# Performance work log

Measured on AMD Instinct MI355X. Metric: run time of the kernel, lower is better.

## Reference

```python
import jax, jax.numpy as jnp
import numpy as np
import math

B, N, D, SEQ = 4, 1024, 512, 256
HID, DIST_D, N_NER, N_LAB = 150, 128, 3, 4
SPANS_PER_WORD = 0.5
ASPECT, OPINION = 1, 2
NUM_DIST_EMB = 512


def setup_inputs() -> dict:
    key = jax.random.key(0)
    ks = jax.random.split(key, 9)
    starts = jax.random.randint(ks[0], (B, N), 0, SEQ)
    widths = jax.random.randint(ks[1], (B, N), 0, 8)
    ends = jnp.clip(starts + widths, 0, SEQ - 1)
    spans = jnp.stack([starts, ends], axis=-1).astype(jnp.int32)  # [B,N,2]
    ner_scores = jax.random.normal(ks[2], (B, N, N_NER), jnp.float32)
    span_embeddings = jax.random.normal(ks[3], (B, N, D), jnp.float32)
    span_mask = jnp.ones((B, N), dtype=bool)

    pair_dim = 2 * D + DIST_D

    def xavier(k, shape):
        std = math.sqrt(2.0 / (shape[0] + shape[1]))
        return jax.random.normal(k, shape, jnp.float32) * std

    dist_table = xavier(ks[4], (NUM_DIST_EMB, DIST_D))
    W1 = xavier(ks[5], (pair_dim, HID)); b1 = jnp.zeros((HID,), jnp.float32)
    W2 = xavier(ks[6], (HID, HID));      b2 = jnp.zeros((HID,), jnp.float32)
    Wc = xavier(ks[7], (HID, N_LAB));    bc = jnp.zeros((N_LAB,), jnp.float32)

    return dict(spans=spans, ner_scores=ner_scores, span_embeddings=span_embeddings,
                span_mask=span_mask, seq_length=SEQ, dist_table=dist_table,
                W1=W1, b1=b1, W2=W2, b2=b2, Wc=Wc, bc=bc)


def bucket_values(d, num_identity=4, num_total=10):
    # semi-logscale buckets: [0,1,2,3,4,5-7,8-15,16-31,32-63,64+]
    logspace = jnp.floor(jnp.log2(jnp.maximum(d, 1).astype(jnp.float32))).astype(jnp.int32) + (num_identity - 1)
    return jnp.clip(jnp.where(d <= num_identity, d, logspace), 0, num_total - 1)


def _prune(scores, mask, k):
    masked = jnp.where(mask, scores, jnp.float32(-1e20))
    _, idx = jax.lax.top_k(masked, k)  # [B,k]
    return idx


def reference(spans, ner_scores, span_embeddings, span_mask, seq_length,
              dist_table, W1, b1, W2, b2, Wc, bc):
    bsz, n_spans, d = span_embeddings.shape
    k = min(int(math.ceil(seq_length * SPANS_PER_WORD)), n_spans)

    a_idx = _prune(ner_scores[..., ASPECT], span_mask, k)    # [B,k]
    o_idx = _prune(ner_scores[..., OPINION], span_mask, k)
    a_keep = jnp.ones((bsz, k), dtype=bool)  # uniform seq_length -> all kept
    o_keep = a_keep

    gather = lambda t, i: jnp.take_along_axis(t, i[..., None], axis=1)
    a_emb = gather(span_embeddings, a_idx)   # [B,k,D]
    o_emb = gather(span_embeddings, o_idx)   # [B,k,D]
    spans_a = gather(spans, a_idx)           # [B,k,2]
    spans_o = gather(spans, o_idx)           # [B,k,2]

    # pairwise min span distance -> bucket -> embedding
    dis1 = jnp.abs(spans_a[..., 0][:, :, None] - spans_o[..., 1][:, None, :])
    dis2 = jnp.abs(spans_a[..., 1][:, :, None] - spans_o[..., 0][:, None, :])
    dis = jnp.minimum(dis1, dis2)                      # [B,k,k]
    dist_emb = dist_table[bucket_values(dis)]          # [B,k,k,DIST_D]

    pair = jnp.concatenate([
        jnp.broadcast_to(a_emb[:, :, None, :], (bsz, k, k, d)),
        jnp.broadcast_to(o_emb[:, None, :, :], (bsz, k, k, d)),
        dist_emb,
    ], axis=-1)                                        # [B,k,k,2D+DIST_D]

    # FeedForward (2 layers, ReLU, dropout=identity at eval) + classifier
    h = jax.nn.relu(pair @ W1 + b1)
    h = jax.nn.relu(h @ W2 + b2)
    scores = h @ Wc + bc                               # [B,k,k,n_labels]

    rel_mask = a_keep[:, :, None] & o_keep[:, None, :]
    return (jax.nn.softmax(scores, axis=-1), rel_mask, pair, spans_a, spans_o)
```

## Files before the change

kernel.cpp:

```cpp
#include <hip/hip_runtime.h>
#include <hip/hip_bf16.h>

#define BB 4
#define NN 1024
#define DD 512
#define KK 128
#define HID 150
#define HIDP 160
#define W2TS 176
#define DIST_D 128
#define PAIRD 1152

typedef __attribute__((ext_vector_type(4))) float f32x4;
typedef __attribute__((ext_vector_type(8))) short s16x8;

__device__ __forceinline__ int bucket_of(int dd) {
    return (dd <= 4) ? dd : min(34 - __clz(dd), 9);
}

__global__ __launch_bounds__(256) void k_topk(const int* __restrict__ spans,
                                              const float* __restrict__ ner,
                                              const float* __restrict__ dist_table,
                                              const float* __restrict__ W1,
                                              const float* __restrict__ b1,
                                              const float* __restrict__ W2,
                                              int* ws_aidx, int* ws_oidx,
                                              int* ws_sa, int* ws_so,
                                              float* ws_cd, __hip_bfloat16* ws_w2t,
                                              float* out3, float* out4) {
    int t = threadIdx.x;
    int bx = blockIdx.x;
    if (bx < 32) {
        __shared__ unsigned long long sk[NN];
        int b = bx >> 3;
        int which = (bx >> 2) & 1;
        int chunk = bx & 3;
        int ch = which ? 2 : 1;
#pragma unroll
        for (int k = 0; k < 4; ++k) {
            int d = k * 256 + t;
            float v = ner[(b * NN + d) * 3 + ch];
            unsigned int u = __float_as_uint(v);
            unsigned int s = (u & 0x80000000u) ? ~u : (u ^ 0x80000000u);
            sk[d] = ((unsigned long long)s << 32) | (unsigned int)(NN - 1 - d);
        }
        __syncthreads();
        int idx = chunk * 256 + t;
        unsigned long long mine = sk[idx];
        int cnt = 0;
#pragma unroll 16
        for (int d = 0; d < NN; ++d) cnt += (sk[d] > mine) ? 1 : 0;
        if (cnt < KK) {
            int s0 = spans[(b * NN + idx) * 2];
            int s1 = spans[(b * NN + idx) * 2 + 1];
            int row = b * KK + cnt;
            if (which == 0) {
                ws_aidx[row] = idx;
                ws_sa[row * 2] = s0; ws_sa[row * 2 + 1] = s1;
                out3[row * 2] = (float)s0; out3[row * 2 + 1] = (float)s1;
            } else {
                ws_oidx[row] = idx;
                ws_so[row * 2] = s0; ws_so[row * 2 + 1] = s1;
                out4[row * 2] = (float)s0; out4[row * 2 + 1] = (float)s1;
            }
        }
    } else if (bx < 42) {
        int bk = bx - 32;
        if (t < HIDP) {
            float acc = 0.f;
            if (t < HID) {
                acc = b1[t];
                for (int d = 0; d < DIST_D; ++d)
                    acc = fmaf(dist_table[bk * DIST_D + d], W1[(size_t)(2 * DD + d) * HID + t], acc);
            }
            ws_cd[bk * HIDP + t] = acc;
        }
    } else {
        int e = (bx - 42) * 256 + t;
        if (e < HIDP * W2TS) {
            int n = e / W2TS, d = e - n * W2TS;
            float v = (n < HID && d < HID) ? W2[d * HID + n] : 0.f;
            ws_w2t[e] = __float2bfloat16(v);
        }
    }
}

__global__ __launch_bounds__(256) void k_prep(const float* __restrict__ emb,
                                              const float* __restrict__ W1,
                                              const int* __restrict__ ws_aidx,
                                              const int* __restrict__ ws_oidx,
                                              float* ws_ca, float* ws_co,
                                              float* ws_acomp, float* ws_ocomp,
                                              float* __restrict__ out1) {
    __shared__ __align__(16) float es[4][DD];
    int t = threadIdx.x;
    int bx = blockIdx.x;

    if (bx >= 384) {
        int i = (bx - 384) * 256 + t;
        ((float4*)out1)[i] = make_float4(1.f, 1.f, 1.f, 1.f);
        return;
    }
    if (bx >= 256) {
        int cb = bx - 256;
        int r0 = cb * 8;
        int c = t & 127;
        bool isA = r0 < 512;
        const int* idxsrc = isA ? ws_aidx : ws_oidx;
        float* dstc = isA ? ws_acomp : ws_ocomp;
        int base = isA ? r0 : r0 - 512;
#pragma unroll
        for (int rr = 0; rr < 8; rr += 2) {
            int brow = base + rr + (t >> 7);
            int b = brow >> 7;
            int idx = idxsrc[brow];
            f32x4 v = ((const f32x4*)(emb + ((size_t)(b * NN) + idx) * DD))[c];
            ((f32x4*)dstc)[(size_t)brow * 128 + c] = v;
        }
        return;
    }

    int which = bx >> 7;
    int row0 = (bx & 127) * 4;
    const int* idxsrc = which ? ws_oidx : ws_aidx;
    for (int x = t; x < 512; x += 256) {
        int r = x >> 7, c = x & 127;
        int row = row0 + r;
        int b = row >> 7;
        int idx = idxsrc[row];
        ((float4*)es[r])[c] = ((const float4*)(emb + ((size_t)(b * NN) + idx) * DD))[c];
    }
    __syncthreads();
    if (t < HIDP) {
        float a0 = 0.f, a1 = 0.f, a2 = 0.f, a3 = 0.f;
        if (t < HID) {
            const float* w = W1 + (size_t)(which * DD) * HID + t;
#pragma unroll 4
            for (int d4 = 0; d4 < 128; ++d4) {
                float4 e0 = ((const float4*)es[0])[d4];
                float4 e1 = ((const float4*)es[1])[d4];
                float4 e2 = ((const float4*)es[2])[d4];
                float4 e3 = ((const float4*)es[3])[d4];
                float w0 = w[(size_t)(4 * d4 + 0) * HID];
                float w1v = w[(size_t)(4 * d4 + 1) * HID];
                float w2v = w[(size_t)(4 * d4 + 2) * HID];
                float w3 = w[(size_t)(4 * d4 + 3) * HID];
                a0 = fmaf(e0.x, w0, a0); a0 = fmaf(e0.y, w1v, a0); a0 = fmaf(e0.z, w2v, a0); a0 = fmaf(e0.w, w3, a0);
                a1 = fmaf(e1.x, w0, a1); a1 = fmaf(e1.y, w1v, a1); a1 = fmaf(e1.z, w2v, a1); a1 = fmaf(e1.w, w3, a1);
                a2 = fmaf(e2.x, w0, a2); a2 = fmaf(e2.y, w1v, a2); a2 = fmaf(e2.z, w2v, a2); a2 = fmaf(e2.w, w3, a2);
                a3 = fmaf(e3.x, w0, a3); a3 = fmaf(e3.y, w1v, a3); a3 = fmaf(e3.z, w2v, a3); a3 = fmaf(e3.w, w3, a3);
            }
        }
        float* dstb = which ? ws_co : ws_ca;
        dstb[(row0 + 0) * HIDP + t] = a0;
        dstb[(row0 + 1) * HIDP + t] = a1;
        dstb[(row0 + 2) * HIDP + t] = a2;
        dstb[(row0 + 3) * HIDP + t] = a3;
    }
}

__global__ __launch_bounds__(256, 2) void k_fused(const float* __restrict__ dist_table,
                                                  const float* __restrict__ Wc,
                                                  const float* __restrict__ bcp,
                                                  const float* __restrict__ b2p,
                                                  const int* __restrict__ ws_sa,
                                                  const int* __restrict__ ws_so,
                                                  const float* __restrict__ ws_ca,
                                                  const float* __restrict__ ws_co,
                                                  const float* __restrict__ ws_cd,
                                                  const __hip_bfloat16* __restrict__ ws_w2t,
                                                  const float* __restrict__ ws_acomp,
                                                  const float* __restrict__ ws_ocomp,
                                                  float* __restrict__ out0,
                                                  float* __restrict__ out2) {
    int t = threadIdx.x;
    int bx = blockIdx.x;

    if (bx & 1) {
        int pid = bx >> 1;
        int b = pid >> 7;
        int ig = (pid >> 2) & 31;
        int jc = pid & 3;
        int i0 = ig << 2;
        int j0 = jc << 5;
        int c = t & 127;
        int half = t >> 7;

        const f32x4* abase = (const f32x4*)ws_acomp;
        const f32x4* obase = (const f32x4*)ws_ocomp;

        f32x4 areg[4];
#pragma unroll
        for (int ii = 0; ii < 4; ++ii)
            areg[ii] = abase[(size_t)(b * KK + i0 + ii) * 128 + c];

        f32x4 oreg[16];
#pragma unroll
        for (int it = 0; it < 16; ++it) {
            int j = it * 2 + half;
            oreg[it] = obase[(size_t)(b * KK + j0 + j) * 128 + c];
        }

        int dj[4], dc[4], so0v[4], so1v[4];
#pragma unroll
        for (int it = 0; it < 4; ++it) {
            int x = it * 256 + t;
            dj[it] = x >> 5; dc[it] = x & 31;
            so0v[it] = ws_so[(b * KK + j0 + dj[it]) * 2];
            so1v[it] = ws_so[(b * KK + j0 + dj[it]) * 2 + 1];
        }
        f32x4 dreg[4][4];
#pragma unroll
        for (int ii = 0; ii < 4; ++ii) {
            int sa0 = ws_sa[(b * KK + i0 + ii) * 2];
            int sa1 = ws_sa[(b * KK + i0 + ii) * 2 + 1];
#pragma unroll
            for (int it = 0; it < 4; ++it) {
                int bkt = bucket_of(min(abs(sa0 - so1v[it]), abs(sa1 - so0v[it])));
                dreg[ii][it] = ((const f32x4*)dist_table)[bkt * 32 + dc[it]];
            }
        }

#pragma unroll
        for (int ii = 0; ii < 4; ++ii) {
            f32x4* dst = (f32x4*)(out2 + (size_t)(b * KK + i0 + ii) * (KK * PAIRD))
                         + (size_t)j0 * 288;
#pragma unroll
            for (int it = 0; it < 16; ++it) {
                int j = it * 2 + half;
                dst[j * 288 + c] = areg[ii];
                dst[j * 288 + 128 + c] = oreg[it];
            }
#pragma unroll
            for (int it = 0; it < 4; ++it)
                dst[dj[it] * 288 + 256 + dc[it]] = dreg[ii][it];
        }
        return;
    }

    int bi = bx >> 1;
    int b = bi >> 7;
    int wave = t >> 6, l = t & 63;
    int lc = l & 15, lg = l >> 4;
    int r0 = wave * 32 + lc, r1 = r0 + 16;

    int sa0 = ws_sa[bi * 2], sa1 = ws_sa[bi * 2 + 1];
    int so00 = ws_so[(b * KK + r0) * 2], so01 = ws_so[(b * KK + r0) * 2 + 1];
    int so10 = ws_so[(b * KK + r1) * 2], so11 = ws_so[(b * KK + r1) * 2 + 1];
    int bkt0 = bucket_of(min(abs(sa0 - so01), abs(sa1 - so00)));
    int bkt1 = bucket_of(min(abs(sa0 - so11), abs(sa1 - so10)));

    const f32x4* ca4 = (const f32x4*)(ws_ca + (size_t)bi * HIDP);
    const f32x4* co04 = (const f32x4*)(ws_co + (size_t)(b * KK + r0) * HIDP);
    const f32x4* co14 = (const f32x4*)(ws_co + (size_t)(b * KK + r1) * HIDP);
    const f32x4* cd04 = (const f32x4*)(ws_cd + (size_t)bkt0 * HIDP);
    const f32x4* cd14 = (const f32x4*)(ws_cd + (size_t)bkt1 * HIDP);

    s16x8 af0[5], af1[5];
    union U8 { s16x8 frag; __hip_bfloat16 h[8]; };
#pragma unroll
    for (int kk = 0; kk < 5; ++kk) {
        int o = kk * 8 + lg * 2;
        f32x4 caa = ca4[o], cab = ca4[o + 1];
        f32x4 s0a = caa + co04[o] + cd04[o];
        f32x4 s0b = cab + co04[o + 1] + cd04[o + 1];
        f32x4 s1a = caa + co14[o] + cd14[o];
        f32x4 s1b = cab + co14[o + 1] + cd14[o + 1];
        U8 u0, u1;
#pragma unroll
        for (int e = 0; e < 4; ++e) {
            u0.h[e]     = __float2bfloat16(fmaxf(s0a[e], 0.f));
            u0.h[e + 4] = __float2bfloat16(fmaxf(s0b[e], 0.f));
            u1.h[e]     = __float2bfloat16(fmaxf(s1a[e], 0.f));
            u1.h[e + 4] = __float2bfloat16(fmaxf(s1b[e], 0.f));
        }
        af0[kk] = u0.frag;
        af1[kk] = u1.frag;
    }

    f32x4 acc[2][10];
#pragma unroll
    for (int mi = 0; mi < 2; ++mi)
#pragma unroll
        for (int nt = 0; nt < 10; ++nt)
            acc[mi][nt] = (f32x4){0.f, 0.f, 0.f, 0.f};

#pragma unroll
    for (int kk = 0; kk < 5; ++kk) {
#pragma unroll
        for (int nt = 0; nt < 10; ++nt) {
            s16x8 bf = *(const s16x8*)&ws_w2t[(nt * 16 + lc) * W2TS + kk * 32 + lg * 8];
            acc[0][nt] = __builtin_amdgcn_mfma_f32_16x16x32_bf16(af0[kk], bf, acc[0][nt], 0, 0, 0);
            acc[1][nt] = __builtin_amdgcn_mfma_f32_16x16x32_bf16(af1[kk], bf, acc[1][nt], 0, 0, 0);
        }
    }

    float4 wcv[10];
    float b2v[10];
#pragma unroll
    for (int nt = 0; nt < 10; ++nt) {
        int n = nt * 16 + lc;
        if (n < HID) {
            wcv[nt] = *(const float4*)(Wc + n * 4);
            b2v[nt] = b2p[n];
        } else {
            wcv[nt] = make_float4(0.f, 0.f, 0.f, 0.f);
            b2v[nt] = 0.f;
        }
    }
    float bc0 = bcp[0], bc1 = bcp[1], bc2 = bcp[2], bc3 = bcp[3];

#pragma unroll
    for (int mi = 0; mi < 2; ++mi) {
#pragma unroll
        for (int r = 0; r < 4; ++r) {
            int j = wave * 32 + mi * 16 + lg * 4 + r;
            float p0 = 0.f, p1 = 0.f, p2 = 0.f, p3 = 0.f;
#pragma unroll
            for (int nt = 0; nt < 10; ++nt) {
                float h2 = fmaxf(acc[mi][nt][r] + b2v[nt], 0.f);
                p0 = fmaf(h2, wcv[nt].x, p0);
                p1 = fmaf(h2, wcv[nt].y, p1);
                p2 = fmaf(h2, wcv[nt].z, p2);
                p3 = fmaf(h2, wcv[nt].w, p3);
            }
#pragma unroll
            for (int m = 8; m >= 1; m >>= 1) {
                p0 += __shfl_xor(p0, m, 16);
                p1 += __shfl_xor(p1, m, 16);
                p2 += __shfl_xor(p2, m, 16);
                p3 += __shfl_xor(p3, m, 16);
            }
            p0 += bc0; p1 += bc1; p2 += bc2; p3 += bc3;
            float mx = fmaxf(fmaxf(p0, p1), fmaxf(p2, p3));
            float e0 = expf(p0 - mx), e1 = expf(p1 - mx), e2 = expf(p2 - mx), e3 = expf(p3 - mx);
            float inv = 1.f / (e0 + e1 + e2 + e3);
            if (lc < 4) {
                float v = (lc == 0) ? e0 : (lc == 1) ? e1 : (lc == 2) ? e2 : e3;
                out0[((size_t)bi * KK + j) * 4 + lc] = v * inv;
            }
        }
    }
}

extern "C" void kernel_launch(void* const* d_in, const int* in_sizes, int n_in,
                              void* d_out, int out_size, void* d_ws, size_t ws_size,
                              hipStream_t stream) {
    const int*   spans = (const int*)d_in[0];
    const float* ner   = (const float*)d_in[1];
    const float* emb   = (const float*)d_in[2];
    const float* dist_table = (const float*)d_in[5];
    const float* W1 = (const float*)d_in[6];
    const float* b1 = (const float*)d_in[7];
    const float* W2 = (const float*)d_in[8];
    const float* b2 = (const float*)d_in[9];
    const float* Wc = (const float*)d_in[10];
    const float* bc = (const float*)d_in[11];

    float* out0 = (float*)d_out;
    float* out1 = out0 + (size_t)BB * KK * KK * 4;
    float* out2 = out1 + (size_t)BB * KK * KK;
    float* out3 = out2 + (size_t)BB * KK * KK * PAIRD;
    float* out4 = out3 + (size_t)BB * KK * 2;

    float* ws_acomp = (float*)d_ws;
    float* ws_ocomp = ws_acomp + 512 * 512;
    int* ws_aidx = (int*)(ws_ocomp + 512 * 512);
    int* ws_oidx = ws_aidx + BB * KK;
    int* ws_sa   = ws_oidx + BB * KK;
    int* ws_so   = ws_sa + BB * KK * 2;
    float* ws_ca = (float*)(ws_so + BB * KK * 2);
    float* ws_co = ws_ca + BB * KK * HIDP;
    float* ws_cd = ws_co + BB * KK * HIDP;
    __hip_bfloat16* ws_w2t = (__hip_bfloat16*)(ws_cd + 16 * HIDP);

    k_topk<<<152, 256, 0, stream>>>(spans, ner, dist_table, W1, b1, W2,
                                    ws_aidx, ws_oidx, ws_sa, ws_so,
                                    ws_cd, ws_w2t, out3, out4);
    k_prep<<<448, 256, 0, stream>>>(emb, W1, ws_aidx, ws_oidx,
                                    ws_ca, ws_co, ws_acomp, ws_ocomp, out1);
    k_fused<<<1024, 256, 0, stream>>>(dist_table, Wc, bc, b2,
                                      ws_sa, ws_so, ws_ca, ws_co, ws_cd, ws_w2t,
                                      ws_acomp, ws_ocomp, out0, out2);
}
```

Measured before the change: 96.99 us.

## Precompute distance buckets and flatten pair-tensor writes into strided grid loop

The distance bucket for every (i,j) pair is now computed once in k_prep blocks and stored in a workspace array. The pair-tensor writer in k_fused becomes a flat grid-stride loop in which each thread writes consecutive float4s. Element coordinates are recovered with multiply-shift division by 9. Writer blocks are interleaved 4:1 with MLP blocks (2560 blocks) instead of 1:1. The aim is fully coalesced streaming stores for the large pair output and better overlap with compute, at the cost of redundant, less-cached reads of the a/o/dist rows and per-element index arithmetic.

```diff
diff --git a/kernel.cpp b/kernel.cpp
--- a/kernel.cpp
+++ b/kernel.cpp
@@ -17,6 +17,8 @@
 __device__ __forceinline__ int bucket_of(int dd) {
     return (dd <= 4) ? dd : min(34 - __clz(dd), 9);
 }
+
+__device__ __forceinline__ int div9(int x) { return (x * 7282) >> 16; }
 
 __global__ __launch_bounds__(256) void k_topk(const int* __restrict__ spans,
                                               const float* __restrict__ ner,
@@ -89,16 +91,32 @@
                                               const float* __restrict__ W1,
                                               const int* __restrict__ ws_aidx,
                                               const int* __restrict__ ws_oidx,
+                                              const int* __restrict__ ws_sa,
+                                              const int* __restrict__ ws_so,
                                               float* ws_ca, float* ws_co,
                                               float* ws_acomp, float* ws_ocomp,
+                                              int* ws_bkt,
                                               float* __restrict__ out1) {
     __shared__ __align__(16) float es[4][DD];
     int t = threadIdx.x;
     int bx = blockIdx.x;
 
+    if (bx >= 448) {
+        int i = (bx - 448) * 256 + t;
+        ((float4*)out1)[i] = make_float4(1.f, 1.f, 1.f, 1.f);
+        return;
+    }
     if (bx >= 384) {
-        int i = (bx - 384) * 256 + t;
-        ((float4*)out1)[i] = make_float4(1.f, 1.f, 1.f, 1.f);
+        int cb = bx - 384;
+#pragma unroll
+        for (int k = 0; k < 4; ++k) {
+            int e = cb * 1024 + k * 256 + t;
+            int bi = e >> 7, j = e & 127;
+            int b = bi >> 7;
+            int sa0 = ws_sa[bi * 2], sa1 = ws_sa[bi * 2 + 1];
+            int so0 = ws_so[(b * KK + j) * 2], so1 = ws_so[(b * KK + j) * 2 + 1];
+            ws_bkt[e] = bucket_of(min(abs(sa0 - so1), abs(sa1 - so0)));
+        }
         return;
     }
     if (bx >= 256) {
@@ -171,74 +189,37 @@
                                                   const __hip_bfloat16* __restrict__ ws_w2t,
                                                   const float* __restrict__ ws_acomp,
                                                   const float* __restrict__ ws_ocomp,
+                                                  const int* __restrict__ ws_bkt,
                                                   float* __restrict__ out0,
                                                   float* __restrict__ out2) {
     int t = threadIdx.x;
     int bx = blockIdx.x;
 
-    if (bx & 1) {
-        int pid = bx >> 1;
-        int b = pid >> 7;
-        int ig = (pid >> 2) & 31;
-        int jc = pid & 3;
-        int i0 = ig << 2;
-        int j0 = jc << 5;
-        int c = t & 127;
-        int half = t >> 7;
-
+    if (bx % 5 != 0) {
+        int pid = bx - bx / 5 - 1;
+        int tid = (pid << 8) + t;
         const f32x4* abase = (const f32x4*)ws_acomp;
         const f32x4* obase = (const f32x4*)ws_ocomp;
-
-        f32x4 areg[4];
-#pragma unroll
-        for (int ii = 0; ii < 4; ++ii)
-            areg[ii] = abase[(size_t)(b * KK + i0 + ii) * 128 + c];
-
-        f32x4 oreg[16];
-#pragma unroll
-        for (int it = 0; it < 16; ++it) {
-            int j = it * 2 + half;
-            oreg[it] = obase[(size_t)(b * KK + j0 + j) * 128 + c];
-        }
-
-        int dj[4], dc[4], so0v[4], so1v[4];
-#pragma unroll
-        for (int it = 0; it < 4; ++it) {
-            int x = it * 256 + t;
-            dj[it] = x >> 5; dc[it] = x & 31;
-            so0v[it] = ws_so[(b * KK + j0 + dj[it]) * 2];
-            so1v[it] = ws_so[(b * KK + j0 + dj[it]) * 2 + 1];
-        }
-        f32x4 dreg[4][4];
-#pragma unroll
-        for (int ii = 0; ii < 4; ++ii) {
-            int sa0 = ws_sa[(b * KK + i0 + ii) * 2];
-            int sa1 = ws_sa[(b * KK + i0 + ii) * 2 + 1];
-#pragma unroll
-            for (int it = 0; it < 4; ++it) {
-                int bkt = bucket_of(min(abs(sa0 - so1v[it]), abs(sa1 - so0v[it])));
-                dreg[ii][it] = ((const f32x4*)dist_table)[bkt * 32 + dc[it]];
-            }
-        }
-
-#pragma unroll
-        for (int ii = 0; ii < 4; ++ii) {
-            f32x4* dst = (f32x4*)(out2 + (size_t)(b * KK + i0 + ii) * (KK * PAIRD))
-                         + (size_t)j0 * 288;
-#pragma unroll
-            for (int it = 0; it < 16; ++it) {
-                int j = it * 2 + half;
-                dst[j * 288 + c] = areg[ii];
-                dst[j * 288 + 128 + c] = oreg[it];
-            }
-#pragma unroll
-            for (int it = 0; it < 4; ++it)
-                dst[dj[it] * 288 + 256 + dc[it]] = dreg[ii][it];
+        const f32x4* dbase = (const f32x4*)dist_table;
+        f32x4* o2 = (f32x4*)out2;
+#pragma unroll 4
+        for (int k = 0; k < 36; ++k) {
+            int f = tid + k * 524288;
+            int bi = div9(f >> 12);
+            int rem = f - bi * 36864;
+            int j = div9(rem >> 5);
+            int s = rem - j * 288;
+            int b = bi >> 7;
+            f32x4 v;
+            if (s < 128)      v = abase[(size_t)bi * 128 + s];
+            else if (s < 256) v = obase[(size_t)(b * KK + j) * 128 + (s - 128)];
+            else              v = dbase[ws_bkt[bi * 128 + j] * 32 + (s - 256)];
+            o2[f] = v;
         }
         return;
     }
 
-    int bi = bx >> 1;
+    int bi = bx / 5;
     int b = bi >> 7;
     int wave = t >> 6, l = t & 63;
     int lc = l & 15, lg = l >> 4;
@@ -365,7 +346,8 @@
 
     float* ws_acomp = (float*)d_ws;
     float* ws_ocomp = ws_acomp + 512 * 512;
-    int* ws_aidx = (int*)(ws_ocomp + 512 * 512);
+    int* ws_bkt  = (int*)(ws_ocomp + 512 * 512);
+    int* ws_aidx = ws_bkt + 512 * KK;
     int* ws_oidx = ws_aidx + BB * KK;
     int* ws_sa   = ws_oidx + BB * KK;
     int* ws_so   = ws_sa + BB * KK * 2;
@@ -377,9 +359,9 @@
     k_topk<<<152, 256, 0, stream>>>(spans, ner, dist_table, W1, b1, W2,
                                     ws_aidx, ws_oidx, ws_sa, ws_so,
                                     ws_cd, ws_w2t, out3, out4);
-    k_prep<<<448, 256, 0, stream>>>(emb, W1, ws_aidx, ws_oidx,
-                                    ws_ca, ws_co, ws_acomp, ws_ocomp, out1);
-    k_fused<<<1024, 256, 0, stream>>>(dist_table, Wc, bc, b2,
+    k_prep<<<512, 256, 0, stream>>>(emb, W1, ws_aidx, ws_oidx, ws_sa, ws_so,
+                                    ws_ca, ws_co, ws_acomp, ws_ocomp, ws_bkt, out1);
+    k_fused<<<2560, 256, 0, stream>>>(dist_table, Wc, bc, b2,
                                       ws_sa, ws_so, ws_ca, ws_co, ws_cd, ws_w2t,
-                                      ws_acomp, ws_ocomp, out0, out2);
-}
+                                      ws_acomp, ws_ocomp, ws_bkt, out0, out2);
+}
```

Result: slower. 111.5 us (+14.9%).
